# Kernel tuning notes

Hardware: AMD Instinct MI355X
Metric: run time of the kernel (lower is better)

Reference implementation:

```python
import jax, jax.numpy as jnp
import numpy as np

B, S, D, H, E = 2, 2048, 1024, 16, 8
DH = D // H
CAP_FACTOR = 1.2


def setup_inputs() -> dict:
    key = jax.random.key(0)
    ks = jax.random.split(key, 14)
    s = 0.02
    return {
        "embed": jax.random.normal(ks[0], (B, S, D), jnp.float32),
        "Wq": jax.random.normal(ks[1], (H, DH, D), jnp.float32) * s,
        "bq": jnp.zeros((H, DH), jnp.float32),
        "Wk": jax.random.normal(ks[2], (H, DH, D), jnp.float32) * s,
        "bk": jnp.zeros((H, DH), jnp.float32),
        "Wv": jax.random.normal(ks[3], (H, DH, D), jnp.float32) * s,
        "bv": jnp.zeros((H, DH), jnp.float32),
        "We": jax.random.normal(ks[4], (E, D, D), jnp.float32) * s,
        "be": jnp.zeros((E, D), jnp.float32),
        "Wsw": jax.random.normal(ks[5], (E, D), jnp.float32) * s,
        "bsw": jnp.zeros((E,), jnp.float32),
        "gamma": jnp.ones((D,), jnp.float32),
        "beta": jnp.zeros((D,), jnp.float32),
    }


def _forward(embed, Wq, bq, Wk, bk, Wv, bv, We, be, Wsw, bsw, gamma, beta):
    b, s, d = embed.shape
    h, e = Wq.shape[0], We.shape[0]
    # --- multi-head attention (all heads batched via einsum) ---
    q = jnp.einsum('bsd,hed->bhse', embed, Wq) + bq[None, :, None, :]
    k = jnp.einsum('bsd,hed->bhse', embed, Wk) + bk[None, :, None, :]
    v = jnp.einsum('bsd,hed->bhse', embed, Wv) + bv[None, :, None, :]
    att = jnp.einsum('bhse,bhte->bhst', q, k)  # [b,h,s,s]
    tril = jnp.tril(jnp.ones((s, s), bool))
    # faithful: upper triangle zeroed (NOT -inf), scale by sqrt(embedding_dim)
    att = jnp.where(tril, att, 0.0) / jnp.sqrt(jnp.float32(d))
    att = jax.nn.softmax(att, axis=-1)
    out = jnp.einsum('bhst,bhte->bhse', att, v)
    hiddens = out.transpose(0, 2, 1, 3).reshape(b, s, d)
    # --- SwitchLinear: top-1 token-choice routing with capacity drop ---
    x = hiddens.reshape(-1, d)  # [N, d]
    n = b * s
    capacity = int(CAP_FACTOR * n / e)
    logits = x @ Wsw.T + bsw
    probs = jax.nn.softmax(logits, axis=-1)
    route_probs = jnp.max(probs, axis=-1)
    routes = jnp.argmax(probs, axis=-1)
    onehot = jax.nn.one_hot(routes, e, dtype=jnp.int32)
    pos = jnp.cumsum(onehot, axis=0) - 1  # position within chosen expert
    pos = jnp.take_along_axis(pos, routes[:, None], axis=1)[:, 0]
    kept = pos < capacity
    slot = jnp.where(kept, routes * capacity + pos, e * capacity)  # overflow row
    dispatch = jnp.zeros((e * capacity + 1, d), x.dtype).at[slot].set(x)
    expert_in = dispatch[: e * capacity].reshape(e, capacity, d)
    expert_out = jnp.einsum('ecd,efd->ecf', expert_in, We) + be[:, None, :]
    expert_flat = jnp.concatenate(
        [expert_out.reshape(e * capacity, d), jnp.zeros((1, d), x.dtype)], 0)
    gathered = expert_flat[slot]
    y = jnp.where(kept[:, None], gathered, x)  # dropped tokens pass through
    y = (y * route_probs[:, None]).reshape(b, s, d)
    # --- residual + LayerNorm ---
    x2 = y + embed
    mean = jnp.mean(x2, axis=-1, keepdims=True)
    var = jnp.var(x2, axis=-1, keepdims=True)
    return (x2 - mean) / jnp.sqrt(var + 1e-5) * gamma + beta


def reference(embed, Wq, bq, Wk, bk, Wv, bv, We, be, Wsw, bsw, gamma, beta):
    return _forward(embed, Wq, bq, Wk, bk, Wv, bv, We, be, Wsw, bsw, gamma, beta)
```

## Files before the change

kernel.cpp:

```cpp
#include <hip/hip_runtime.h>

constexpr int B = 2, S = 2048, D = 1024, H = 16, E = 8, DH = 64;
constexpr int N = B * S;
constexpr int CAP = 614;
constexpr int ECAP = 640;
constexpr float INV_SQRT_D = 0.03125f;

typedef __bf16 bf16x8 __attribute__((ext_vector_type(8)));
typedef float f32x4 __attribute__((ext_vector_type(4)));

__device__ __forceinline__ ushort f2bf(float x) {
  __bf16 h = (__bf16)x;
  return __builtin_bit_cast(unsigned short, h);
}
__device__ __forceinline__ float bf2f(ushort u) {
  __bf16 h = __builtin_bit_cast(__bf16, u);
  return (float)h;
}
__device__ __forceinline__ void gld16(const void* g, void* l) {
  __builtin_amdgcn_global_load_lds(
      (const __attribute__((address_space(1))) unsigned int*)g,
      (__attribute__((address_space(3))) unsigned int*)l, 16, 0, 0);
}

__global__ __launch_bounds__(256) void cvt_pair(const float* __restrict__ in,
                                                ushort* __restrict__ out)
{
  const long long idx4 = (long long)blockIdx.x * 256 + threadIdx.x;
  const float4 xv = ((const float4*)in)[idx4];
  const long long row = idx4 >> 8;
  const int col = (int)((idx4 & 255) << 2);
  float xs[4] = {xv.x, xv.y, xv.z, xv.w};
  ushort4 hi, lo;
  ushort* hp = (ushort*)&hi; ushort* lp = (ushort*)&lo;
  #pragma unroll
  for (int c = 0; c < 4; ++c) {
    ushort h = f2bf(xs[c]);
    hp[c] = h;
    lp[c] = f2bf(xs[c] - bf2f(h));
  }
  *(ushort4*)&out[row * 2048 + col] = hi;
  *(ushort4*)&out[row * 2048 + 1024 + col] = lo;
}

__global__ __launch_bounds__(256) void cvt_plain(const float* __restrict__ in,
                                                 ushort* __restrict__ out)
{
  const long long idx4 = (long long)blockIdx.x * 256 + threadIdx.x;
  const float4 xv = ((const float4*)in)[idx4];
  ushort4 o;
  o.x = f2bf(xv.x); o.y = f2bf(xv.y); o.z = f2bf(xv.z); o.w = f2bf(xv.w);
  *(ushort4*)&out[idx4 * 4] = o;
}

template <bool TRIPLE, int EPI>
__global__ __launch_bounds__(256) void mfma_gemm(
    const ushort* __restrict__ A, const ushort* __restrict__ W,
    const float* __restrict__ b0, const float* __restrict__ b1,
    const float* __restrict__ b2, float* __restrict__ C,
    ushort* __restrict__ pairout,
    long long strideA, long long strideW, long long strideC,
    long long biasStride, int biasSel)
{
  constexpr int KA = TRIPLE ? 2048 : 1024;
  constexpr int KW = TRIPLE ? 2048 : 1024;
  constexpr int NSTEP = TRIPLE ? 48 : 16;
  const int z = blockIdx.z;
  A += (long long)z * strideA;
  W += (long long)z * strideW;
  C += (long long)z * strideC;
  const float* bp = biasSel ? (z == 0 ? b0 : (z == 1 ? b1 : b2))
                            : b0 + (long long)z * biasStride;

  __shared__ char smem[32768] __attribute__((aligned(128)));
  const int tid = threadIdx.x;
  const int lane = tid & 63;
  const int lrow = lane & 15;
  const int lk = lane >> 4;
  const int wv = tid >> 6;
  const int rAc = (wv >> 1) * 64;
  const int rBc = (wv & 1) * 64;
  const int bm0 = blockIdx.y * 128;
  const int bn0 = blockIdx.x * 128;
  const int srow = tid >> 3;
  const int su = tid & 7;

  f32x4 acc[4][4] = {};

  for (int step = 0; step < NSTEP; ++step) {
    const int k0 = step * 64;
    int srcA, srcB;
    if (TRIPLE) {
      srcA = (k0 < 2048) ? k0 : k0 - 2048;
      srcB = (k0 < 1024) ? k0 : k0 - 1024;
    } else { srcA = k0; srcB = k0; }
    __syncthreads();
    #pragma unroll
    for (int i = 0; i < 4; ++i) {
      const int row = i * 32 + srow;
      const int u = su ^ (row & 7);
      gld16(A + (long long)(bm0 + row) * KA + srcA + u * 8,
            smem + i * 4096 + wv * 1024);
      gld16(W + (long long)(bn0 + row) * KW + srcB + u * 8,
            smem + 16384 + i * 4096 + wv * 1024);
    }
    asm volatile("s_waitcnt vmcnt(0)" ::: "memory");
    __syncthreads();
    #pragma unroll
    for (int h = 0; h < 2; ++h) {
      bf16x8 af[4], bfr[4];
      #pragma unroll
      for (int i = 0; i < 4; ++i) {
        const int row = rAc + i * 16 + lrow;
        const int u = (h * 4 + lk) ^ (row & 7);
        af[i] = *(const bf16x8*)(smem + row * 128 + u * 16);
      }
      #pragma unroll
      for (int j = 0; j < 4; ++j) {
        const int row = rBc + j * 16 + lrow;
        const int u = (h * 4 + lk) ^ (row & 7);
        bfr[j] = *(const bf16x8*)(smem + 16384 + row * 128 + u * 16);
      }
      #pragma unroll
      for (int i = 0; i < 4; ++i)
        #pragma unroll
        for (int j = 0; j < 4; ++j)
          acc[i][j] = __builtin_amdgcn_mfma_f32_16x16x32_bf16(
              af[i], bfr[j], acc[i][j], 0, 0, 0);
    }
  }
  const int rg = (lane >> 4) * 4;
  #pragma unroll
  for (int j = 0; j < 4; ++j) {
    const int col = bn0 + rBc + j * 16 + (lane & 15);
    const float bj = bp[col];
    #pragma unroll
    for (int i = 0; i < 4; ++i) {
      const int rbase = bm0 + rAc + i * 16 + rg;
      if constexpr (EPI == 0) {
        #pragma unroll
        for (int r = 0; r < 4; ++r)
          C[(long long)(rbase + r) * 1024 + col] = acc[i][j][r] + bj;
      } else {
        const int hh = col >> 6, e = col & 63;
        const int b = rbase >> 11;
        if (z < 2) {
          const int sbase = rbase & 2047;
          ushort* dst = pairout + (long long)z * 8388608 +
                        ((long long)(b * 16 + hh) * 2048 + sbase) * 128 + e;
          #pragma unroll
          for (int r = 0; r < 4; ++r) {
            float val = acc[i][j][r] + bj;
            ushort vh = f2bf(val);
            dst[r * 128] = vh;
            dst[r * 128 + 64] = f2bf(val - bf2f(vh));
          }
        } else {
          const int tb = rbase & 2047;
          ushort4 hi4, lo4;
          ushort* hp = (ushort*)&hi4; ushort* lp = (ushort*)&lo4;
          #pragma unroll
          for (int r = 0; r < 4; ++r) {
            float val = acc[i][j][r] + bj;
            ushort vh = f2bf(val);
            hp[r] = vh;
            lp[r] = f2bf(val - bf2f(vh));
          }
          ushort* vdst = pairout + 2ll * 8388608 +
                         (long long)(b * 16 + hh) * 262144 +
                         (long long)e * 2048 + tb;
          *(ushort4*)vdst = hi4;
          *(ushort4*)(vdst + 131072) = lo4;
        }
      }
    }
  }
}

__global__ __launch_bounds__(256) void suffix_kernel(const ushort* __restrict__ vtp,
                                                     float* __restrict__ vsuf)
{
  const int R = blockIdx.x;
  const int bh = R >> 6, e = R & 63;
  const ushort* hi = vtp + (long long)bh * 262144 + (long long)e * 2048;
  const ushort* lo = hi + 131072;
  const int tid = threadIdx.x;
  ushort4 h0 = *(const ushort4*)(hi + tid * 8);
  ushort4 h1 = *(const ushort4*)(hi + tid * 8 + 4);
  ushort4 l0 = *(const ushort4*)(lo + tid * 8);
  ushort4 l1 = *(const ushort4*)(lo + tid * 8 + 4);
  float v[8];
  v[0] = bf2f(h0.x) + bf2f(l0.x); v[1] = bf2f(h0.y) + bf2f(l0.y);
  v[2] = bf2f(h0.z) + bf2f(l0.z); v[3] = bf2f(h0.w) + bf2f(l0.w);
  v[4] = bf2f(h1.x) + bf2f(l1.x); v[5] = bf2f(h1.y) + bf2f(l1.y);
  v[6] = bf2f(h1.z) + bf2f(l1.z); v[7] = bf2f(h1.w) + bf2f(l1.w);
  float s = 0.f;
  #pragma unroll
  for (int x = 0; x < 8; ++x) s += v[x];
  __shared__ float ss[256];
  ss[tid] = s;
  __syncthreads();
  for (int off = 1; off < 256; off <<= 1) {
    float t = (tid + off < 256) ? ss[tid + off] : 0.f;
    __syncthreads();
    ss[tid] += t;
    __syncthreads();
  }
  float acc = (tid < 255) ? ss[tid + 1] : 0.f;
  float out[8];
  for (int x = 7; x >= 0; --x) { acc += v[x]; out[x] = acc; }
  #pragma unroll
  for (int x = 0; x < 8; ++x)
    vsuf[(long long)R * 2048 + tid * 8 + x] = out[x];
}

__global__ __launch_bounds__(256) void attn_mfma(
    const ushort* __restrict__ qp, const ushort* __restrict__ kp,
    const ushort* __restrict__ vtp, const float* __restrict__ vsuf,
    float* __restrict__ hid)
{
  const int bh = blockIdx.y;
  const int s0 = (int)(gridDim.x - 1 - blockIdx.x) * 64;
  const int tid = threadIdx.x;
  const int lane = tid & 63;
  const int wv = tid >> 6;
  const int g = lane >> 4, c = lane & 15;

  __shared__ char smem[66944] __attribute__((aligned(16)));
  ushort* qs = (ushort*)smem;
  ushort* ks = (ushort*)(smem + 16384);
  ushort* vt = (ushort*)(smem + 32768);
  float*  wl = (float*)(smem + 49152);

  const ushort* qbase = qp + (long long)bh * 2048 * 128;
  const ushort* kbase = kp + (long long)bh * 2048 * 128;
  const ushort* vbase = vtp + (long long)bh * 262144;

  #pragma unroll
  for (int i = 0; i < 4; ++i) {
    const int L = i * 256 + tid;
    const int row = L >> 4, u = L & 15;
    const int us = u ^ (row & 15);
    gld16(qbase + (long long)(s0 + row) * 128 + us * 8,
          smem + i * 4096 + wv * 1024);
  }

  f32x4 oacc[4] = {};
  float l_acc[4] = {};

  for (int t0 = 0; t0 <= s0; t0 += 64) {
    __syncthreads();
    #pragma unroll
    for (int i = 0; i < 4; ++i) {
      const int L = i * 256 + tid;
      const int row = L >> 4, u = L & 15;
      const int us = u ^ (row & 15);
      gld16(kbase + (long long)(t0 + row) * 128 + us * 8,
            smem + 16384 + i * 4096 + wv * 1024);
    }
    #pragma unroll
    for (int i = 0; i < 4; ++i) {
      const int L = i * 256 + tid;
      const int sec = L >> 9, row = (L >> 3) & 63, u = L & 7;
      const int us = u ^ (row & 7);
      gld16(vbase + (long long)sec * 131072 + (long long)row * 2048 + t0 + us * 8,
            smem + 32768 + i * 4096 + wv * 1024);
    }
    asm volatile("s_waitcnt vmcnt(0)" ::: "memory");
    __syncthreads();

    f32x4 acc[4] = {};
    #pragma unroll
    for (int h = 0; h < 2; ++h) {
      const int qrow = wv * 16 + c;
      bf16x8 qh = *(const bf16x8*)(qs + qrow * 128 + (((h * 4 + g) ^ (qrow & 15)) * 8));
      bf16x8 ql = *(const bf16x8*)(qs + qrow * 128 + (((8 + h * 4 + g) ^ (qrow & 15)) * 8));
      #pragma unroll
      for (int j = 0; j < 4; ++j) {
        const int krow = j * 16 + c;
        bf16x8 kh = *(const bf16x8*)(ks + krow * 128 + (((h * 4 + g) ^ (krow & 15)) * 8));
        bf16x8 kl = *(const bf16x8*)(ks + krow * 128 + (((8 + h * 4 + g) ^ (krow & 15)) * 8));
        acc[j] = __builtin_amdgcn_mfma_f32_16x16x32_bf16(qh, kh, acc[j], 0, 0, 0);
        acc[j] = __builtin_amdgcn_mfma_f32_16x16x32_bf16(ql, kh, acc[j], 0, 0, 0);
        acc[j] = __builtin_amdgcn_mfma_f32_16x16x32_bf16(qh, kl, acc[j], 0, 0, 0);
      }
    }

    float prt[4] = {0.f, 0.f, 0.f, 0.f};
    #pragma unroll
    for (int j = 0; j < 4; ++j) {
      #pragma unroll
      for (int r = 0; r < 4; ++r) {
        const int sg = s0 + wv * 16 + 4 * g + r;
        const int tg = t0 + j * 16 + c;
        const float w = (tg <= sg) ? __expf(acc[j][r] * INV_SQRT_D) : 0.f;
        wl[(wv * 16 + 4 * g + r) * 68 + j * 16 + c] = w;
        prt[r] += w;
      }
    }
    #pragma unroll
    for (int off = 1; off < 16; off <<= 1)
      #pragma unroll
      for (int r = 0; r < 4; ++r) prt[r] += __shfl_xor(prt[r], off);
    #pragma unroll
    for (int r = 0; r < 4; ++r) l_acc[r] += prt[r];

    __syncthreads();

    #pragma unroll
    for (int h = 0; h < 2; ++h) {
      const int wrow = wv * 16 + c;
      const float4 w0 = *(const float4*)&wl[wrow * 68 + h * 32 + g * 8];
      const float4 w1 = *(const float4*)&wl[wrow * 68 + h * 32 + g * 8 + 4];
      const float wf[8] = {w0.x, w0.y, w0.z, w0.w, w1.x, w1.y, w1.z, w1.w};
      bf16x8 wh, wlo;
      #pragma unroll
      for (int x = 0; x < 8; ++x) {
        __bf16 hh = (__bf16)wf[x];
        wh[x] = hh;
        wlo[x] = (__bf16)(wf[x] - (float)hh);
      }
      #pragma unroll
      for (int j = 0; j < 4; ++j) {
        const int vrow = j * 16 + c;
        bf16x8 vh = *(const bf16x8*)(vt + vrow * 64 + (((h * 4 + g) ^ (vrow & 7)) * 8));
        bf16x8 vl = *(const bf16x8*)(vt + 4096 + vrow * 64 + (((h * 4 + g) ^ (vrow & 7)) * 8));
        oacc[j] = __builtin_amdgcn_mfma_f32_16x16x32_bf16(wh, vh, oacc[j], 0, 0, 0);
        oacc[j] = __builtin_amdgcn_mfma_f32_16x16x32_bf16(wlo, vh, oacc[j], 0, 0, 0);
        oacc[j] = __builtin_amdgcn_mfma_f32_16x16x32_bf16(wh, vl, oacc[j], 0, 0, 0);
      }
    }
  }

  const int b = bh >> 4, hh = bh & 15;
  #pragma unroll
  for (int r = 0; r < 4; ++r) {
    const int sg = s0 + wv * 16 + 4 * g + r;
    const float denom = l_acc[r] + (float)(S - 1 - sg);
    #pragma unroll
    for (int j = 0; j < 4; ++j) {
      const int e = j * 16 + c;
      const float suf = (sg + 1 < S) ? vsuf[((long long)bh * 64 + e) * 2048 + sg + 1] : 0.f;
      hid[(long long)(b * S + sg) * 1024 + hh * 64 + e] = (oacc[j][r] + suf) / denom;
    }
  }
}

__global__ __launch_bounds__(256) void router_kernel(
    const float* __restrict__ x, const float* __restrict__ Wsw,
    const float* __restrict__ bsw, int* __restrict__ routes,
    float* __restrict__ rprob)
{
  const int w = threadIdx.x >> 6, lane = threadIdx.x & 63;
  const int i = blockIdx.x * 4 + w;
  float p[E] = {};
  const float4* xr = (const float4*)(x + (long long)i * D);
  #pragma unroll
  for (int t = 0; t < 4; ++t) {
    float4 xv = xr[lane + 64 * t];
    #pragma unroll
    for (int e = 0; e < E; ++e) {
      float4 wv = ((const float4*)(Wsw + e * D))[lane + 64 * t];
      p[e] += xv.x * wv.x + xv.y * wv.y + xv.z * wv.z + xv.w * wv.w;
    }
  }
  #pragma unroll
  for (int off = 32; off; off >>= 1)
    #pragma unroll
    for (int e = 0; e < E; ++e) p[e] += __shfl_xor(p[e], off);
  if (lane == 0) {
    float m = -1e30f; int arg = 0;
    #pragma unroll
    for (int e = 0; e < E; ++e) {
      float l = p[e] + bsw[e];
      if (l > m) { m = l; arg = e; }
      p[e] = l;
    }
    float sum = 0.f;
    #pragma unroll
    for (int e = 0; e < E; ++e) sum += __expf(p[e] - m);
    routes[i] = arg;
    rprob[i] = 1.f / sum;
  }
}

__global__ __launch_bounds__(256) void scan_kernel(const int* __restrict__ routes,
                                                   int* __restrict__ slot)
{
  __shared__ int hist[256][E];
  const int tid = threadIdx.x;
  const int per = N / 256;
  int cnt[E] = {};
  for (int j = 0; j < per; ++j) cnt[routes[tid * per + j]]++;
  #pragma unroll
  for (int e = 0; e < E; ++e) hist[tid][e] = cnt[e];
  __syncthreads();
  if (tid < E) {
    int run = 0;
    for (int t = 0; t < 256; ++t) { int tmp = hist[t][tid]; hist[t][tid] = run; run += tmp; }
  }
  __syncthreads();
  int run[E];
  #pragma unroll
  for (int e = 0; e < E; ++e) run[e] = hist[tid][e];
  for (int j = 0; j < per; ++j) {
    int i = tid * per + j;
    int r = routes[i];
    int pos = run[r]++;
    slot[i] = (pos < CAP) ? r * ECAP + pos : -1;
  }
}

__global__ __launch_bounds__(256) void dispatch_kernel(
    const float* __restrict__ x, const int* __restrict__ slot,
    ushort* __restrict__ expert_in)
{
  const int i = blockIdx.x;
  const int sl = slot[i];
  if (sl < 0) return;
  float4 xv = ((const float4*)&x[(long long)i * D])[threadIdx.x];
  ushort4 o;
  o.x = f2bf(xv.x); o.y = f2bf(xv.y); o.z = f2bf(xv.z); o.w = f2bf(xv.w);
  ((ushort4*)&expert_in[(long long)sl * D])[threadIdx.x] = o;
}

__global__ __launch_bounds__(256) void finalize_kernel(
    const float* __restrict__ x, const float* __restrict__ eout,
    const int* __restrict__ slot, const float* __restrict__ rprob,
    const float* __restrict__ embed, const float* __restrict__ gamma,
    const float* __restrict__ beta, float* __restrict__ out)
{
  const int i = blockIdx.x;
  const int tid = threadIdx.x;
  const int sl = slot[i];
  const float rp = rprob[i];
  const float4* src = (sl >= 0) ? (const float4*)&eout[(long long)sl * D]
                                : (const float4*)&x[(long long)i * D];
  float4 yv = src[tid];
  float4 ev = ((const float4*)&embed[(long long)i * D])[tid];
  float v0 = yv.x * rp + ev.x;
  float v1 = yv.y * rp + ev.y;
  float v2 = yv.z * rp + ev.z;
  float v3 = yv.w * rp + ev.w;
  float s1 = v0 + v1 + v2 + v3;
  float s2 = v0*v0 + v1*v1 + v2*v2 + v3*v3;
  #pragma unroll
  for (int off = 32; off; off >>= 1) {
    s1 += __shfl_xor(s1, off);
    s2 += __shfl_xor(s2, off);
  }
  __shared__ float wsum[4], wsq[4];
  const int wid = tid >> 6, lid = tid & 63;
  if (lid == 0) { wsum[wid] = s1; wsq[wid] = s2; }
  __syncthreads();
  float tot  = wsum[0] + wsum[1] + wsum[2] + wsum[3];
  float tot2 = wsq[0] + wsq[1] + wsq[2] + wsq[3];
  const float mean = tot * (1.f / D);
  const float var = tot2 * (1.f / D) - mean * mean;
  const float rstd = rsqrtf(var + 1e-5f);
  float4 gv = ((const float4*)gamma)[tid];
  float4 bv = ((const float4*)beta)[tid];
  float4 ov;
  ov.x = (v0 - mean) * rstd * gv.x + bv.x;
  ov.y = (v1 - mean) * rstd * gv.y + bv.y;
  ov.z = (v2 - mean) * rstd * gv.z + bv.z;
  ov.w = (v3 - mean) * rstd * gv.w + bv.w;
  ((float4*)&out[(long long)i * D])[tid] = ov;
}

extern "C" void kernel_launch(void* const* d_in, const int* in_sizes, int n_in,
                              void* d_out, int out_size, void* d_ws, size_t ws_size,
                              hipStream_t stream) {
  const float* embed = (const float*)d_in[0];
  const float* Wq = (const float*)d_in[1];
  const float* bq = (const float*)d_in[2];
  const float* Wk = (const float*)d_in[3];
  const float* bk = (const float*)d_in[4];
  const float* Wv = (const float*)d_in[5];
  const float* bv = (const float*)d_in[6];
  const float* We = (const float*)d_in[7];
  const float* be = (const float*)d_in[8];
  const float* Wsw = (const float*)d_in[9];
  const float* bsw = (const float*)d_in[10];
  const float* gamma = (const float*)d_in[11];
  const float* beta = (const float*)d_in[12];
  float* out = (float*)d_out;

  char* base = (char*)d_ws;
  ushort* epair      = (ushort*)base;
  float*  hid        = (float*)base;
  ushort* wpair      = (ushort*)(base + 16777216);
  ushort* expert_in  = (ushort*)(base + 16777216);
  ushort* pairs      = (ushort*)(base + 29360128);
  float*  expert_out = (float*)(base + 29360128);
  ushort* qp  = pairs;
  ushort* kp  = pairs + 8388608;
  ushort* vtp = pairs + 2 * 8388608;
  float*  vsuf = (float*)(base + 79691776);
  ushort* webf = (ushort*)(base + 79691776);
  int*    routes = (int*)(base + 96468992);
  int*    slot   = routes + N;
  float*  rprob  = (float*)(slot + N);

  cvt_pair<<<N * D / 1024, 256, 0, stream>>>(embed, epair);
  cvt_pair<<<D * D / 1024, 256, 0, stream>>>(Wq, wpair + 0ll * D * 2048);
  cvt_pair<<<D * D / 1024, 256, 0, stream>>>(Wk, wpair + 1ll * D * 2048);
  cvt_pair<<<D * D / 1024, 256, 0, stream>>>(Wv, wpair + 2ll * D * 2048);
  mfma_gemm<true, 1><<<dim3(8, 32, 3), 256, 0, stream>>>(
      epair, wpair, bq, bk, bv, nullptr, pairs,
      0, (long long)D * 2048, 0, 0, 1);
  suffix_kernel<<<B * H * 64, 256, 0, stream>>>(vtp, vsuf);
  attn_mfma<<<dim3(S / 64, B * H), 256, 0, stream>>>(qp, kp, vtp, vsuf, hid);
  router_kernel<<<N / 4, 256, 0, stream>>>(hid, Wsw, bsw, routes, rprob);
  scan_kernel<<<1, 256, 0, stream>>>(routes, slot);
  cvt_plain<<<(int)((long long)E * D * D / 1024), 256, 0, stream>>>(We, webf);
  dispatch_kernel<<<N, 256, 0, stream>>>(hid, slot, expert_in);
  mfma_gemm<false, 0><<<dim3(8, ECAP / 128, E), 256, 0, stream>>>(
      expert_in, webf, be, nullptr, nullptr, expert_out, nullptr,
      (long long)ECAP * D, (long long)D * D, (long long)ECAP * D,
      (long long)D, 0);
  finalize_kernel<<<N, 256, 0, stream>>>(hid, expert_out, slot, rprob,
                                         embed, gamma, beta, out);
}
```

Before: 478.1 us.

## Double-buffer K/V tiles in attention with 128-row query blocks per workgroup

The attention kernel now runs 512 threads (8 waves) per workgroup covering 128 query rows, so each K/V tile loaded into LDS serves twice as many queries. K/V tiles are double-buffered: the next tile is prefetched with async global-to-LDS loads while the current one is computed, using partial vmcnt waits and raw s_barrier in place of full syncthreads. LDS use grows to about 130 KB of dynamic shared memory, which limits occupancy to one workgroup per CU. The diagonal tile now does masked work for more rows, and the hand-written waitcnt counts must exactly match the number of outstanding loads.

```diff
diff --git a/kernel.cpp b/kernel.cpp
--- a/kernel.cpp
+++ b/kernel.cpp
@@ -5,6 +5,7 @@
 constexpr int CAP = 614;
 constexpr int ECAP = 640;
 constexpr float INV_SQRT_D = 0.03125f;
+constexpr int ATTN_LDS = 133120;
 
 typedef __bf16 bf16x8 __attribute__((ext_vector_type(8)));
 typedef float f32x4 __attribute__((ext_vector_type(4)));
@@ -214,23 +215,47 @@
     vsuf[(long long)R * 2048 + tid * 8 + x] = out[x];
 }
 
-__global__ __launch_bounds__(256) void attn_mfma(
+__device__ __forceinline__ void attn_stage_kv(
+    const ushort* kbase, const ushort* vbase, int t0,
+    char* kdst, char* vdst, int tid, int wv)
+{
+  #pragma unroll
+  for (int i = 0; i < 2; ++i) {
+    const int L = i * 512 + tid;
+    const int row = L >> 4, u = L & 15;
+    gld16(kbase + (long long)(t0 + row) * 128 + ((u ^ (row & 15)) * 8),
+          kdst + i * 8192 + wv * 1024);
+  }
+  #pragma unroll
+  for (int i = 0; i < 2; ++i) {
+    const int L = i * 512 + tid;
+    const int sec = L >> 9, vr = (L >> 3) & 63, u = L & 7;
+    gld16(vbase + (long long)sec * 131072 + (long long)vr * 2048 + t0 +
+              ((u ^ (vr & 7)) * 8),
+          vdst + i * 8192 + wv * 1024);
+  }
+}
+
+__global__ __launch_bounds__(512) void attn_mfma(
     const ushort* __restrict__ qp, const ushort* __restrict__ kp,
     const ushort* __restrict__ vtp, const float* __restrict__ vsuf,
     float* __restrict__ hid)
 {
+  extern __shared__ char smem[];
   const int bh = blockIdx.y;
-  const int s0 = (int)(gridDim.x - 1 - blockIdx.x) * 64;
+  const int qi = (int)(gridDim.x - 1 - blockIdx.x);
+  const int sB0 = qi * 128;
   const int tid = threadIdx.x;
   const int lane = tid & 63;
   const int wv = tid >> 6;
   const int g = lane >> 4, c = lane & 15;
 
-  __shared__ char smem[66944] __attribute__((aligned(16)));
   ushort* qs = (ushort*)smem;
-  ushort* ks = (ushort*)(smem + 16384);
-  ushort* vt = (ushort*)(smem + 32768);
-  float*  wl = (float*)(smem + 49152);
+  char* kbuf0 = smem + 32768;
+  char* kbuf1 = smem + 49152;
+  char* vbuf0 = smem + 65536;
+  char* vbuf1 = smem + 81920;
+  float* wl = (float*)(smem + 98304);
 
   const ushort* qbase = qp + (long long)bh * 2048 * 128;
   const ushort* kbase = kp + (long long)bh * 2048 * 128;
@@ -238,41 +263,36 @@
 
   #pragma unroll
   for (int i = 0; i < 4; ++i) {
-    const int L = i * 256 + tid;
+    const int L = i * 512 + tid;
     const int row = L >> 4, u = L & 15;
-    const int us = u ^ (row & 15);
-    gld16(qbase + (long long)(s0 + row) * 128 + us * 8,
-          smem + i * 4096 + wv * 1024);
-  }
+    gld16(qbase + (long long)(sB0 + row) * 128 + ((u ^ (row & 15)) * 8),
+          smem + i * 8192 + wv * 1024);
+  }
+  char* kcur = kbuf0; char* knext = kbuf1;
+  char* vcur = vbuf0; char* vnext = vbuf1;
+  attn_stage_kv(kbase, vbase, 0, kcur, vcur, tid, wv);
 
   f32x4 oacc[4] = {};
   float l_acc[4] = {};
-
-  for (int t0 = 0; t0 <= s0; t0 += 64) {
-    __syncthreads();
-    #pragma unroll
-    for (int i = 0; i < 4; ++i) {
-      const int L = i * 256 + tid;
-      const int row = L >> 4, u = L & 15;
-      const int us = u ^ (row & 15);
-      gld16(kbase + (long long)(t0 + row) * 128 + us * 8,
-            smem + 16384 + i * 4096 + wv * 1024);
-    }
-    #pragma unroll
-    for (int i = 0; i < 4; ++i) {
-      const int L = i * 256 + tid;
-      const int sec = L >> 9, row = (L >> 3) & 63, u = L & 7;
-      const int us = u ^ (row & 7);
-      gld16(vbase + (long long)sec * 131072 + (long long)row * 2048 + t0 + us * 8,
-            smem + 32768 + i * 4096 + wv * 1024);
-    }
-    asm volatile("s_waitcnt vmcnt(0)" ::: "memory");
-    __syncthreads();
+  const int nt = 2 * qi + 2;
+  const int qrow = wv * 16 + c;
+
+  for (int t = 0; t < nt; ++t) {
+    const int t0 = t * 64;
+    if (t + 1 < nt) {
+      attn_stage_kv(kbase, vbase, t0 + 64, knext, vnext, tid, wv);
+      asm volatile("s_waitcnt vmcnt(4)" ::: "memory");
+    } else {
+      asm volatile("s_waitcnt vmcnt(0)" ::: "memory");
+    }
+    __builtin_amdgcn_s_barrier();
+
+    const ushort* ks = (const ushort*)kcur;
+    const ushort* vt = (const ushort*)vcur;
 
     f32x4 acc[4] = {};
     #pragma unroll
     for (int h = 0; h < 2; ++h) {
-      const int qrow = wv * 16 + c;
       bf16x8 qh = *(const bf16x8*)(qs + qrow * 128 + (((h * 4 + g) ^ (qrow & 15)) * 8));
       bf16x8 ql = *(const bf16x8*)(qs + qrow * 128 + (((8 + h * 4 + g) ^ (qrow & 15)) * 8));
       #pragma unroll
@@ -291,7 +311,7 @@
     for (int j = 0; j < 4; ++j) {
       #pragma unroll
       for (int r = 0; r < 4; ++r) {
-        const int sg = s0 + wv * 16 + 4 * g + r;
+        const int sg = sB0 + wv * 16 + 4 * g + r;
         const int tg = t0 + j * 16 + c;
         const float w = (tg <= sg) ? __expf(acc[j][r] * INV_SQRT_D) : 0.f;
         wl[(wv * 16 + 4 * g + r) * 68 + j * 16 + c] = w;
@@ -305,7 +325,8 @@
     #pragma unroll
     for (int r = 0; r < 4; ++r) l_acc[r] += prt[r];
 
-    __syncthreads();
+    asm volatile("s_waitcnt lgkmcnt(0)" ::: "memory");
+    __builtin_amdgcn_s_barrier();
 
     #pragma unroll
     for (int h = 0; h < 2; ++h) {
@@ -330,12 +351,15 @@
         oacc[j] = __builtin_amdgcn_mfma_f32_16x16x32_bf16(wh, vl, oacc[j], 0, 0, 0);
       }
     }
+    __builtin_amdgcn_s_barrier();
+    char* tk = kcur; kcur = knext; knext = tk;
+    char* tv = vcur; vcur = vnext; vnext = tv;
   }
 
   const int b = bh >> 4, hh = bh & 15;
   #pragma unroll
   for (int r = 0; r < 4; ++r) {
-    const int sg = s0 + wv * 16 + 4 * g + r;
+    const int sg = sB0 + wv * 16 + 4 * g + r;
     const float denom = l_acc[r] + (float)(S - 1 - sg);
     #pragma unroll
     for (int j = 0; j < 4; ++j) {
@@ -486,6 +510,10 @@
   const float* beta = (const float*)d_in[12];
   float* out = (float*)d_out;
 
+  (void)hipFuncSetAttribute((const void*)attn_mfma,
+                            hipFuncAttributeMaxDynamicSharedMemorySize,
+                            ATTN_LDS);
+
   char* base = (char*)d_ws;
   ushort* epair      = (ushort*)base;
   float*  hid        = (float*)base;
@@ -510,7 +538,8 @@
       epair, wpair, bq, bk, bv, nullptr, pairs,
       0, (long long)D * 2048, 0, 0, 1);
   suffix_kernel<<<B * H * 64, 256, 0, stream>>>(vtp, vsuf);
-  attn_mfma<<<dim3(S / 64, B * H), 256, 0, stream>>>(qp, kp, vtp, vsuf, hid);
+  attn_mfma<<<dim3(S / 128, B * H), 512, ATTN_LDS, stream>>>(
+      qp, kp, vtp, vsuf, hid);
   router_kernel<<<N / 4, 256, 0, stream>>>(hid, Wsw, bsw, routes, rprob);
   scan_kernel<<<1, 256, 0, stream>>>(routes, slot);
   cvt_plain<<<(int)((long long)E * D * D / 1024), 256, 0, stream>>>(We, webf);
```

New measurement: 469.3 us. Within noise of the previous version (-1.9%).
